# Kernel tuning notes

Measured on AMD Instinct MI355X. Metric: run time of the kernel, lower is better.

## Reference

```python
import jax, jax.numpy as jnp
import numpy as np

N_NODES = 100000
N_EDGES = 1200000
D_FEAT = 64
D_OUT = 128


def setup_inputs() -> dict:
    key = jax.random.key(0)
    k1, k2, k3, k4, k5, k6 = jax.random.split(key, 6)
    hk = jax.random.normal(k1, (N_NODES, D_FEAT), dtype=jnp.float32)
    hu = jax.random.normal(k2, (N_NODES, D_FEAT), dtype=jnp.float32)
    W = jax.random.normal(k3, (D_OUT, D_FEAT), dtype=jnp.float32) * 0.05
    b = jax.random.normal(k4, (D_OUT,), dtype=jnp.float32) * 0.05
    src = jax.random.randint(k5, (N_EDGES,), 0, N_NODES, dtype=jnp.int64)
    dst = jax.random.randint(k6, (N_EDGES,), 0, N_NODES, dtype=jnp.int64)
    return {"hk": hk, "hu": hu, "W": W, "b": b, "src": src, "dst": dst}


def reference(hk, hu, W, b, src, dst):
    n = hk.shape[0]
    # u_dot_v: per-edge score = <hk[src], hu[dst]>  -> [E]
    scores = jnp.sum(hk[src] * hu[dst], axis=-1)
    # edge_softmax: softmax over edges grouped by destination node
    seg_max = jax.ops.segment_max(scores, dst, num_segments=n)  # [N]
    ex = jnp.exp(scores - seg_max[dst])                          # [E]
    seg_sum = jax.ops.segment_sum(ex, dst, num_segments=n)      # [N]
    alpha = ex / seg_sum[dst]                                    # [E]
    # u_mul_e_sum: weighted scatter-aggregate of source features into dst
    rst = jax.ops.segment_sum(hk[src] * alpha[:, None], dst, num_segments=n)  # [N, D]
    # fc + relu
    return jax.nn.relu(rst @ W.T + b)
```

## Files before the change

kernel.cpp:

```cpp
#include <hip/hip_runtime.h>
#include <math.h>

#define D_FEAT 64
#define D_OUT  128

__global__ void k_count(const int* __restrict__ dst, int* __restrict__ deg, int E) {
    int e = blockIdx.x * blockDim.x + threadIdx.x;
    if (e >= E) return;
    atomicAdd(deg + dst[e], 1);
}

__global__ __launch_bounds__(256) void k_scan_a(const int* __restrict__ deg,
                                                int* __restrict__ rowptr,
                                                int* __restrict__ partials, int N) {
    __shared__ int wsum[4];
    const int t = threadIdx.x;
    const int base = blockIdx.x * 1024 + t * 4;
    int v0 = (base + 0 < N) ? deg[base + 0] : 0;
    int v1 = (base + 1 < N) ? deg[base + 1] : 0;
    int v2 = (base + 2 < N) ? deg[base + 2] : 0;
    int v3 = (base + 3 < N) ? deg[base + 3] : 0;
    int lsum = v0 + v1 + v2 + v3;
    int x = lsum;
#pragma unroll
    for (int off = 1; off < 64; off <<= 1) {
        int y = __shfl_up(x, off);
        if ((t & 63) >= off) x += y;
    }
    const int wid = t >> 6;
    if ((t & 63) == 63) wsum[wid] = x;
    __syncthreads();
    int woff = 0;
    for (int w = 0; w < wid; ++w) woff += wsum[w];
    int run = woff + x - lsum;
    if (base + 0 < N) rowptr[base + 0] = run; run += v0;
    if (base + 1 < N) rowptr[base + 1] = run; run += v1;
    if (base + 2 < N) rowptr[base + 2] = run; run += v2;
    if (base + 3 < N) rowptr[base + 3] = run;
    if (t == 0) partials[blockIdx.x] = wsum[0] + wsum[1] + wsum[2] + wsum[3];
}

__global__ __launch_bounds__(128) void k_scan_b(int* __restrict__ partials, int NB) {
    __shared__ int buf[128];
    const int t = threadIdx.x;
    const int orig = (t < NB) ? partials[t] : 0;
    buf[t] = orig;
    __syncthreads();
#pragma unroll
    for (int off = 1; off < 128; off <<= 1) {
        int v = (t >= off) ? buf[t - off] : 0;
        __syncthreads();
        buf[t] += v;
        __syncthreads();
    }
    if (t < NB) partials[t] = buf[t] - orig;
}

__global__ __launch_bounds__(256) void k_scan_c(int* __restrict__ rowptr,
                                                int* __restrict__ cursor,
                                                const int* __restrict__ partials,
                                                int N, int E) {
    const int t = threadIdx.x;
    const int base = blockIdx.x * 1024 + t * 4;
    const int add = partials[blockIdx.x];
#pragma unroll
    for (int i = 0; i < 4; ++i) {
        if (base + i < N) {
            int v = rowptr[base + i] + add;
            rowptr[base + i] = v;
            cursor[base + i] = v;
        }
    }
    if (blockIdx.x == 0 && t == 0) rowptr[N] = E;
}

__global__ void k_fill(const int* __restrict__ src, const int* __restrict__ dst,
                       int* __restrict__ cursor, int* __restrict__ srcs, int E) {
    int e = blockIdx.x * blockDim.x + threadIdx.x;
    if (e >= E) return;
    int pos = atomicAdd(cursor + dst[e], 1);
    srcs[pos] = src[e];
}

__global__ __launch_bounds__(256) void k_agg(const float* __restrict__ hk,
                                             const float* __restrict__ hu,
                                             const int* __restrict__ rowptr,
                                             const int* __restrict__ srcs,
                                             float* __restrict__ rst, int N) {
    const int tid = blockIdx.x * blockDim.x + threadIdx.x;
    const int n = tid >> 6;
    if (n >= N) return;
    const int lane = tid & 63;
    const int q = lane & 15;
    const int g = lane >> 4;

    const int beg = rowptr[n];
    const int end = rowptr[n + 1];

    const float4 hv = *reinterpret_cast<const float4*>(hu + (size_t)n * D_FEAT + q * 4);

    float m = -INFINITY, s = 0.f;
    float4 acc = make_float4(0.f, 0.f, 0.f, 0.f);

    for (int p = beg + g; p < end; p += 4) {
        const int sidx = srcs[p];
        const float4 a = *reinterpret_cast<const float4*>(hk + (size_t)sidx * D_FEAT + q * 4);
        float dsc = a.x * hv.x + a.y * hv.y + a.z * hv.z + a.w * hv.w;
        dsc += __shfl_xor(dsc, 1);
        dsc += __shfl_xor(dsc, 2);
        dsc += __shfl_xor(dsc, 4);
        dsc += __shfl_xor(dsc, 8);
        const float mn = fmaxf(m, dsc);
        const float sc = __expf(m - mn);
        const float pe = __expf(dsc - mn);
        s = s * sc + pe;
        acc.x = acc.x * sc + pe * a.x;
        acc.y = acc.y * sc + pe * a.y;
        acc.z = acc.z * sc + pe * a.z;
        acc.w = acc.w * sc + pe * a.w;
        m = mn;
    }

#pragma unroll
    for (int off = 16; off <= 32; off <<= 1) {
        const float m2 = __shfl_xor(m, off);
        const float s2 = __shfl_xor(s, off);
        const float ax = __shfl_xor(acc.x, off);
        const float ay = __shfl_xor(acc.y, off);
        const float az = __shfl_xor(acc.z, off);
        const float aw = __shfl_xor(acc.w, off);
        const float mn = fmaxf(m, m2);
        const float sc1 = (m == mn) ? 1.f : __expf(m - mn);
        const float sc2 = (m2 == mn) ? 1.f : __expf(m2 - mn);
        s = s * sc1 + s2 * sc2;
        acc.x = acc.x * sc1 + ax * sc2;
        acc.y = acc.y * sc1 + ay * sc2;
        acc.z = acc.z * sc1 + az * sc2;
        acc.w = acc.w * sc1 + aw * sc2;
        m = mn;
    }

    if (g == 0) {
        float4 o;
        if (end > beg) {
            const float inv = 1.f / s;
            o = make_float4(acc.x * inv, acc.y * inv, acc.z * inv, acc.w * inv);
        } else {
            o = make_float4(0.f, 0.f, 0.f, 0.f);
        }
        *reinterpret_cast<float4*>(rst + (size_t)n * D_FEAT + q * 4) = o;
    }
}

__global__ __launch_bounds__(64) void k_fc(const float* __restrict__ rst,
                                           const float* __restrict__ W,
                                           const float* __restrict__ b,
                                           float* __restrict__ out, int N) {
    __shared__ float lds[64 * 33];
    const int lane = (int)threadIdx.x;
    const int n0 = (int)(blockIdx.x >> 2) * 64;
    const int o0 = (int)(blockIdx.x & 3) * 32;
    const int n = n0 + lane;

    float4 r[16];
    if (n < N) {
        const float4* rp = reinterpret_cast<const float4*>(rst + (size_t)n * D_FEAT);
#pragma unroll
        for (int i = 0; i < 16; ++i) r[i] = rp[i];
    } else {
#pragma unroll
        for (int i = 0; i < 16; ++i) r[i] = make_float4(0.f, 0.f, 0.f, 0.f);
    }

#pragma unroll
    for (int g = 0; g < 8; ++g) {
        const int o = o0 + g * 4;
        const float* w0 = W + (size_t)o * D_FEAT;
        const float* w1 = w0 + D_FEAT;
        const float* w2 = w0 + 2 * D_FEAT;
        const float* w3 = w0 + 3 * D_FEAT;
        float a0 = b[o + 0];
        float a1 = b[o + 1];
        float a2 = b[o + 2];
        float a3 = b[o + 3];
#pragma unroll
        for (int k4 = 0; k4 < 16; ++k4) {
            const float4 rv = r[k4];
            const int k = k4 * 4;
            a0 += rv.x * w0[k] + rv.y * w0[k + 1] + rv.z * w0[k + 2] + rv.w * w0[k + 3];
            a1 += rv.x * w1[k] + rv.y * w1[k + 1] + rv.z * w1[k + 2] + rv.w * w1[k + 3];
            a2 += rv.x * w2[k] + rv.y * w2[k + 1] + rv.z * w2[k + 2] + rv.w * w2[k + 3];
            a3 += rv.x * w3[k] + rv.y * w3[k + 1] + rv.z * w3[k + 2] + rv.w * w3[k + 3];
        }
        lds[lane * 33 + g * 4 + 0] = fmaxf(a0, 0.f);
        lds[lane * 33 + g * 4 + 1] = fmaxf(a1, 0.f);
        lds[lane * 33 + g * 4 + 2] = fmaxf(a2, 0.f);
        lds[lane * 33 + g * 4 + 3] = fmaxf(a3, 0.f);
    }
    __syncthreads();

    const int rrow = lane >> 3;
    const int c = (lane & 7) * 4;
#pragma unroll
    for (int j = 0; j < 8; ++j) {
        const int rr = j * 8 + rrow;
        const int nn = n0 + rr;
        if (nn < N) {
            const float* lp = lds + rr * 33 + c;
            float4 v = make_float4(lp[0], lp[1], lp[2], lp[3]);
            *reinterpret_cast<float4*>(out + (size_t)nn * D_OUT + o0 + c) = v;
        }
    }
}

extern "C" void kernel_launch(void* const* d_in, const int* in_sizes, int n_in,
                              void* d_out, int out_size, void* d_ws, size_t ws_size,
                              hipStream_t stream) {
    const float* hk = (const float*)d_in[0];
    const float* hu = (const float*)d_in[1];
    const float* W  = (const float*)d_in[2];
    const float* b  = (const float*)d_in[3];
    const int* src  = (const int*)d_in[4];
    const int* dst  = (const int*)d_in[5];

    const int N = in_sizes[0] / D_FEAT;
    const int E = in_sizes[4];

    auto pad16 = [](size_t x) { return (x + 15) & ~(size_t)15; };
    size_t o_rowptr = 0;
    size_t o_deg    = pad16(o_rowptr + N + 1);
    size_t o_cursor = o_deg + pad16(N);
    size_t o_srcs   = o_cursor + pad16(N);
    size_t o_part   = o_srcs + pad16(E);
    size_t o_rst    = o_part + 128;

    int* rowptr   = (int*)d_ws + o_rowptr;
    int* deg      = (int*)d_ws + o_deg;
    int* cursor   = (int*)d_ws + o_cursor;
    int* srcs     = (int*)d_ws + o_srcs;
    int* partials = (int*)d_ws + o_part;
    float* rst    = (float*)d_ws + o_rst;

    hipMemsetAsync(deg, 0, pad16(N) * sizeof(int), stream);

    const int B = 256;
    const int g_edge = (E + B - 1) / B;
    const int NB = (N + 1023) / 1024;

    k_count<<<g_edge, B, 0, stream>>>(dst, deg, E);
    k_scan_a<<<NB, 256, 0, stream>>>(deg, rowptr, partials, N);
    k_scan_b<<<1, 128, 0, stream>>>(partials, NB);
    k_scan_c<<<NB, 256, 0, stream>>>(rowptr, cursor, partials, N, E);
    k_fill<<<g_edge, B, 0, stream>>>(src, dst, cursor, srcs, E);
    k_agg<<<(N + 3) / 4, 256, 0, stream>>>(hk, hu, rowptr, srcs, rst, N);
    k_fc<<<((N + 63) / 64) * 4, 64, 0, stream>>>(rst, W, b, (float*)d_out, N);
}
```

Before: 350.1 us.

## Partition CSR fill by destination range across block groups

Result: faster. 322.5 us (-7.9%).

```diff
diff --git a/kernel.cpp b/kernel.cpp
--- a/kernel.cpp
+++ b/kernel.cpp
@@ -74,12 +74,32 @@
     if (blockIdx.x == 0 && t == 0) rowptr[N] = E;
 }
 
-__global__ void k_fill(const int* __restrict__ src, const int* __restrict__ dst,
-                       int* __restrict__ cursor, int* __restrict__ srcs, int E) {
-    int e = blockIdx.x * blockDim.x + threadIdx.x;
-    if (e >= E) return;
-    int pos = atomicAdd(cursor + dst[e], 1);
-    srcs[pos] = src[e];
+__global__ __launch_bounds__(256) void k_fill(const int* __restrict__ src,
+                                              const int* __restrict__ dst,
+                                              int* __restrict__ cursor,
+                                              int* __restrict__ srcs,
+                                              int E, int N) {
+    const int pid = (int)(blockIdx.x & 7);
+    const int cb  = (int)(blockIdx.x >> 3);
+    const int cpp = (int)(gridDim.x >> 3);
+    const int lo = (int)(((long long)pid * N) / 8);
+    const int hi = (int)(((long long)(pid + 1) * N) / 8);
+
+    const int nq = E >> 2;
+    const int stride = cpp * 256;
+    for (int q = cb * 256 + (int)threadIdx.x; q < nq; q += stride) {
+        const int4 d4 = reinterpret_cast<const int4*>(dst)[q];
+        const int e0 = q * 4;
+        if (d4.x >= lo && d4.x < hi) { int pos = atomicAdd(cursor + d4.x, 1); srcs[pos] = src[e0 + 0]; }
+        if (d4.y >= lo && d4.y < hi) { int pos = atomicAdd(cursor + d4.y, 1); srcs[pos] = src[e0 + 1]; }
+        if (d4.z >= lo && d4.z < hi) { int pos = atomicAdd(cursor + d4.z, 1); srcs[pos] = src[e0 + 2]; }
+        if (d4.w >= lo && d4.w < hi) { int pos = atomicAdd(cursor + d4.w, 1); srcs[pos] = src[e0 + 3]; }
+    }
+    if (cb == 0 && (int)threadIdx.x < (E & 3)) {
+        int e = nq * 4 + (int)threadIdx.x;
+        int d = dst[e];
+        if (d >= lo && d < hi) { int pos = atomicAdd(cursor + d, 1); srcs[pos] = src[e]; }
+    }
 }
 
 __global__ __launch_bounds__(256) void k_agg(const float* __restrict__ hk,
@@ -251,7 +271,7 @@
     k_scan_a<<<NB, 256, 0, stream>>>(deg, rowptr, partials, N);
     k_scan_b<<<1, 128, 0, stream>>>(partials, NB);
     k_scan_c<<<NB, 256, 0, stream>>>(rowptr, cursor, partials, N, E);
-    k_fill<<<g_edge, B, 0, stream>>>(src, dst, cursor, srcs, E);
+    k_fill<<<2048, 256, 0, stream>>>(src, dst, cursor, srcs, E, N);
     k_agg<<<(N + 3) / 4, 256, 0, stream>>>(hk, hu, rowptr, srcs, rst, N);
     k_fc<<<((N + 63) / 64) * 4, 64, 0, stream>>>(rst, W, b, (float*)d_out, N);
 }
```
